# Optimization experiments

Measured on AMD Instinct MI355X. Metric: run time of the kernel, lower is better.

Reference implementation:

```python
import jax, jax.numpy as jnp
import numpy as np

LDDT_THRESHOLDS = jnp.array([0.5, 1.0, 2.0, 4.0], dtype=jnp.float32)
NUCLEIC_ACID_CUTOFF = 30.0
OTHER_CUTOFF = 15.0


def _cdist(x):
    # pairwise euclidean distances, safe sqrt (zero grad on diagonal zeros)
    sq = jnp.sum(x * x, axis=-1)                      # [b, n]
    d2 = sq[:, :, None] + sq[:, None, :] - 2.0 * jnp.einsum('bic,bjc->bij', x, x)
    d2 = jnp.maximum(d2, 0.0)
    pos = d2 > 0.0
    return jnp.where(pos, jnp.sqrt(jnp.where(pos, d2, 1.0)), 0.0)


def setup_inputs() -> dict:
    key = jax.random.key(0)
    k1, k2, k3, k4, k5 = jax.random.split(key, 5)
    b, n = 2, 4096
    true_coords = jax.random.normal(k1, (b, n, 3), dtype=jnp.float32) * 10.0
    pred_coords = true_coords + jax.random.normal(k2, (b, n, 3), dtype=jnp.float32) * 1.0
    is_dna = jax.random.bernoulli(k3, 0.25, (b, n))
    is_rna = jax.random.bernoulli(k4, 0.25, (b, n))
    coords_mask = jax.random.bernoulli(k5, 0.9, (b, n))
    return {
        'pred_coords': pred_coords,
        'true_coords': true_coords,
        'is_dna': is_dna,
        'is_rna': is_rna,
        'coords_mask': coords_mask,
    }


def reference(pred_coords, true_coords, is_dna, is_rna, coords_mask):
    b, n, _ = pred_coords.shape
    pred_dists = _cdist(pred_coords)                  # [b, n, n]
    true_dists = _cdist(true_coords)                  # [b, n, n]
    dist_diff = jnp.abs(true_dists - pred_dists)      # [b, n, n]

    # sigmoid(threshold - dist_diff), averaged over the 4 thresholds
    eps = jax.nn.sigmoid(LDDT_THRESHOLDS - dist_diff[..., None]).mean(axis=-1)  # [b, n, n]

    is_nucleotide = is_dna | is_rna                   # [b, n]
    nuc_pair = is_nucleotide[:, :, None] & is_nucleotide[:, None, :]
    inclusion_radius = jnp.where(nuc_pair,
                                 true_dists < NUCLEIC_ACID_CUTOFF,
                                 true_dists < OTHER_CUTOFF)
    mask = inclusion_radius & ~jnp.eye(n, dtype=bool)[None]
    paired_coords_mask = coords_mask[:, :, None] & coords_mask[:, None, :]
    mask = mask & paired_coords_mask

    maskf = mask.astype(eps.dtype)
    num = jnp.sum(eps * maskf, axis=(-1, -2))         # [b]
    den = jnp.maximum(jnp.sum(maskf, axis=(-1, -2)), 1.0)
    lddt = num / den
    return 1.0 - lddt.mean()
```

## Files before the change

### kernel.cpp

```cpp
#include <hip/hip_runtime.h>
#include <math.h>

#define N      4096
#define BLOCK  256
#define SEG    64
#define NITILE (N / BLOCK)
#define NJSEG  (N / SEG)
#define NTILE_TRI 544

#define PN0 4.0f
#define PN1 3.384183069f
#define PN2 0.750655861f
#define PN3 0.036699475f
#define PD1 1.128061023f
#define PD2 0.375327930f
#define PD3 0.036699475f
#define PD4 0.000553084f

__device__ __forceinline__ int tri_offset(int t) { return 66 * t - 2 * t * t; }

__global__ __launch_bounds__(BLOCK, 6) void lddt_main_kernel(
    const float* __restrict__ pred, const float* __restrict__ truec,
    const int* __restrict__ is_dna, const int* __restrict__ is_rna,
    const int* __restrict__ cmask, float* __restrict__ ws)
{
    const int L     = blockIdx.x;
    const int batch = blockIdx.z;
    const int tid   = threadIdx.x;

    int itile = 0;
#pragma unroll
    for (int u = 1; u < NITILE; ++u) itile += (L >= tri_offset(u)) ? 1 : 0;
    const int jseg = 4 * itile + (L - tri_offset(itile));
    const bool diag = (jseg >> 2) == itile;

    const int i = itile * BLOCK + tid;

    const float* pb = pred  + (size_t)batch * N * 3;
    const float* tb = truec + (size_t)batch * N * 3;
    const int* dnab = is_dna + (size_t)batch * N;
    const int* rnab = is_rna + (size_t)batch * N;
    const int* cmb  = cmask  + (size_t)batch * N;

    __shared__ float4 jP[SEG], jT[SEG];
    const int j0 = jseg * SEG;
    if (tid < SEG) {
        const int j = j0 + tid;
        jP[tid] = make_float4(pb[j*3+0], pb[j*3+1], pb[j*3+2],
                              (dnab[j] | rnab[j]) ? 15.0f : 0.0f);
        jT[tid] = make_float4(tb[j*3+0], tb[j*3+1], tb[j*3+2],
                              cmb[j] ? 1.0f : 0.0f);
    }
    __syncthreads();

    const float pix = pb[i*3+0], piy = pb[i*3+1], piz = pb[i*3+2];
    const float tix = tb[i*3+0], tiy = tb[i*3+1], tiz = tb[i*3+2];
    const float inuc01 = (dnab[i] | rnab[i]) ? 1.0f : 0.0f;
    const float icm    = cmb[i] ? 1.0f : 0.0f;

    float num = 0.0f, den = 0.0f;

#define PAIR_BODY(JJ, NEED_TRI)                                                \
    {                                                                          \
        const float4 P = jP[JJ];                                               \
        const float4 T = jT[JJ];                                               \
        float dxp = pix - P.x, dyp = piy - P.y, dzp = piz - P.z;               \
        float d2p = fmaf(dxp, dxp, fmaf(dyp, dyp, dzp * dzp));                 \
        float dp  = __builtin_amdgcn_sqrtf(d2p);                               \
        float dxt = tix - T.x, dyt = tiy - T.y, dzt = tiz - T.z;               \
        float d2t = fmaf(dxt, dxt, fmaf(dyt, dyt, dzt * dzt));                 \
        float dt  = __builtin_amdgcn_sqrtf(d2t);                               \
        float dd = fminf(fabsf(dt - dp), 20.0f);                               \
        float e  = __expf(dd);                                                 \
        float nN = fmaf(e, fmaf(e, fmaf(e, PN3, PN2), PN1), PN0);              \
        float nD = fmaf(e, fmaf(e, fmaf(e, fmaf(e, PD4, PD3), PD2), PD1), 1.0f);\
        float s  = nN * __builtin_amdgcn_rcpf(nD);                             \
        float cutoff = fmaf(inuc01, P.w, 15.0f);                               \
        bool keep = (dt < cutoff);                                             \
        if (NEED_TRI) keep = keep && (j0 + (JJ) > i);                          \
        float m = keep ? T.w : 0.0f;                                           \
        den += m;                                                              \
        num  = fmaf(m, s, num);                                                \
    }

    if (diag) {
#pragma unroll 8
        for (int jj = 0; jj < SEG; ++jj) PAIR_BODY(jj, true)
    } else {
#pragma unroll 8
        for (int jj = 0; jj < SEG; ++jj) PAIR_BODY(jj, false)
    }
#undef PAIR_BODY

    num *= 0.5f * icm;
    den *= 2.0f * icm;

    for (int off = 32; off > 0; off >>= 1) {
        num += __shfl_down(num, off);
        den += __shfl_down(den, off);
    }
    __shared__ float rn[BLOCK / 64], rd[BLOCK / 64];
    const int wid = tid >> 6, lane = tid & 63;
    if (lane == 0) { rn[wid] = num; rd[wid] = den; }
    __syncthreads();
    if (tid == 0) {
        float tn = rn[0] + rn[1] + rn[2] + rn[3];
        float td = rd[0] + rd[1] + rd[2] + rd[3];
        const int bid = batch * NTILE_TRI + L;
        ws[bid * 2 + 0] = tn;
        ws[bid * 2 + 1] = td;
    }
}

__global__ __launch_bounds__(BLOCK) void finalize_kernel(
    const float* __restrict__ ws, float* __restrict__ out, int b)
{
    __shared__ float sn[4], sd[4];
    float acc = 0.0f;
    for (int k = 0; k < b; ++k) {
        float n = 0.0f, d = 0.0f;
        for (int p = threadIdx.x; p < NTILE_TRI; p += BLOCK) {
            n += ws[(k * NTILE_TRI + p) * 2 + 0];
            d += ws[(k * NTILE_TRI + p) * 2 + 1];
        }
        for (int off = 32; off > 0; off >>= 1) {
            n += __shfl_down(n, off);
            d += __shfl_down(d, off);
        }
        if ((threadIdx.x & 63) == 0) { sn[threadIdx.x >> 6] = n; sd[threadIdx.x >> 6] = d; }
        __syncthreads();
        if (threadIdx.x == 0) {
            float tn = sn[0] + sn[1] + sn[2] + sn[3];
            float td = sd[0] + sd[1] + sd[2] + sd[3];
            acc += tn / fmaxf(td, 1.0f);
        }
        __syncthreads();
    }
    if (threadIdx.x == 0) out[0] = 1.0f - acc / (float)b;
}

extern "C" void kernel_launch(void* const* d_in, const int* in_sizes, int n_in,
                              void* d_out, int out_size, void* d_ws, size_t ws_size,
                              hipStream_t stream) {
    const float* pred  = (const float*)d_in[0];
    const float* truec = (const float*)d_in[1];
    const int* is_dna  = (const int*)d_in[2];
    const int* is_rna  = (const int*)d_in[3];
    const int* cmask   = (const int*)d_in[4];
    float* out = (float*)d_out;
    float* ws  = (float*)d_ws;

    const int b = in_sizes[2] / N;

    dim3 grid(NTILE_TRI, 1, b);
    lddt_main_kernel<<<grid, BLOCK, 0, stream>>>(pred, truec, is_dna, is_rna, cmask, ws);
    finalize_kernel<<<1, BLOCK, 0, stream>>>(ws, out, b);
}
```

Before: 86.63 us.

## Pair rcp across two entries, compare squared cutoff, halve j-segment, fuse finalize

Combines two pair sigmoid rationals under one reciprocal by cross-multiplying, which removes one rcp per pair. The radius check now compares squared distances, and the clamp is lowered to 10 to keep the product of denominators in range. The j-segment shrinks to 32, doubling the block count, and occupancy hints rise to 8. The separate finalize kernel is replaced by atomics plus a last-block reduction, with a memset added to zero the accumulators. This adds atomic contention, float atomics that make the sum order nondeterministic, and possible precision loss in the product of denominators.

```diff
diff --git a/kernel.cpp b/kernel.cpp
--- a/kernel.cpp
+++ b/kernel.cpp
@@ -3,10 +3,9 @@
 
 #define N      4096
 #define BLOCK  256
-#define SEG    64
+#define JW     32
 #define NITILE (N / BLOCK)
-#define NJSEG  (N / SEG)
-#define NTILE_TRI 544
+#define NTRI   1088
 
 #define PN0 4.0f
 #define PN1 3.384183069f
@@ -17,12 +16,16 @@
 #define PD3 0.036699475f
 #define PD4 0.000553084f
 
-__device__ __forceinline__ int tri_offset(int t) { return 66 * t - 2 * t * t; }
+#define WS_CTR   0
+#define WS_ACC   16
 
-__global__ __launch_bounds__(BLOCK, 6) void lddt_main_kernel(
+__device__ __forceinline__ int tri_off(int t) { return 132 * t - 4 * t * t; }
+
+__global__ __launch_bounds__(BLOCK, 8) void lddt_main_kernel(
     const float* __restrict__ pred, const float* __restrict__ truec,
     const int* __restrict__ is_dna, const int* __restrict__ is_rna,
-    const int* __restrict__ cmask, float* __restrict__ ws)
+    const int* __restrict__ cmask, float* __restrict__ ws,
+    float* __restrict__ out, int nblk_total, int b)
 {
     const int L     = blockIdx.x;
     const int batch = blockIdx.z;
@@ -30,9 +33,9 @@
 
     int itile = 0;
 #pragma unroll
-    for (int u = 1; u < NITILE; ++u) itile += (L >= tri_offset(u)) ? 1 : 0;
-    const int jseg = 4 * itile + (L - tri_offset(itile));
-    const bool diag = (jseg >> 2) == itile;
+    for (int u = 1; u < NITILE; ++u) itile += (L >= tri_off(u)) ? 1 : 0;
+    const int jseg = 8 * itile + (L - tri_off(itile));
+    const bool diag = (jseg < 8 * itile + 8);
 
     const int i = itile * BLOCK + tid;
 
@@ -42,12 +45,12 @@
     const int* rnab = is_rna + (size_t)batch * N;
     const int* cmb  = cmask  + (size_t)batch * N;
 
-    __shared__ float4 jP[SEG], jT[SEG];
-    const int j0 = jseg * SEG;
-    if (tid < SEG) {
+    __shared__ float4 jP[JW], jT[JW];
+    const int j0 = jseg * JW;
+    if (tid < JW) {
         const int j = j0 + tid;
         jP[tid] = make_float4(pb[j*3+0], pb[j*3+1], pb[j*3+2],
-                              (dnab[j] | rnab[j]) ? 15.0f : 0.0f);
+                              (dnab[j] | rnab[j]) ? 675.0f : 0.0f);
         jT[tid] = make_float4(tb[j*3+0], tb[j*3+1], tb[j*3+2],
                               cmb[j] ? 1.0f : 0.0f);
     }
@@ -60,37 +63,46 @@
 
     float num = 0.0f, den = 0.0f;
 
-#define PAIR_BODY(JJ, NEED_TRI)                                                \
+#define PAIR(K, NEED_TRI, NN, ND, M)                                           \
     {                                                                          \
-        const float4 P = jP[JJ];                                               \
-        const float4 T = jT[JJ];                                               \
+        const float4 P = jP[K];                                                \
+        const float4 T = jT[K];                                                \
         float dxp = pix - P.x, dyp = piy - P.y, dzp = piz - P.z;               \
         float d2p = fmaf(dxp, dxp, fmaf(dyp, dyp, dzp * dzp));                 \
         float dp  = __builtin_amdgcn_sqrtf(d2p);                               \
         float dxt = tix - T.x, dyt = tiy - T.y, dzt = tiz - T.z;               \
         float d2t = fmaf(dxt, dxt, fmaf(dyt, dyt, dzt * dzt));                 \
         float dt  = __builtin_amdgcn_sqrtf(d2t);                               \
-        float dd = fminf(fabsf(dt - dp), 20.0f);                               \
-        float e  = __expf(dd);                                                 \
-        float nN = fmaf(e, fmaf(e, fmaf(e, PN3, PN2), PN1), PN0);              \
-        float nD = fmaf(e, fmaf(e, fmaf(e, fmaf(e, PD4, PD3), PD2), PD1), 1.0f);\
-        float s  = nN * __builtin_amdgcn_rcpf(nD);                             \
-        float cutoff = fmaf(inuc01, P.w, 15.0f);                               \
-        bool keep = (dt < cutoff);                                             \
-        if (NEED_TRI) keep = keep && (j0 + (JJ) > i);                          \
-        float m = keep ? T.w : 0.0f;                                           \
-        den += m;                                                              \
-        num  = fmaf(m, s, num);                                                \
+        float dd  = fminf(fabsf(dt - dp), 10.0f);                              \
+        float e   = __expf(dd);                                                \
+        NN = fmaf(e, fmaf(e, fmaf(e, PN3, PN2), PN1), PN0);                    \
+        ND = fmaf(e, fmaf(e, fmaf(e, fmaf(e, PD4, PD3), PD2), PD1), 1.0f);     \
+        float cutsq = fmaf(inuc01, P.w, 225.0f);                               \
+        bool keep = (d2t < cutsq);                                             \
+        if (NEED_TRI) keep = keep && (j0 + (K) > i);                           \
+        M = keep ? T.w : 0.0f;                                                 \
+    }
+
+#define PAIR2(JJ, NEED_TRI)                                                    \
+    {                                                                          \
+        float n1, d1, m1, n2, d2, m2;                                          \
+        PAIR(JJ, NEED_TRI, n1, d1, m1)                                         \
+        PAIR((JJ) + 1, NEED_TRI, n2, d2, m2)                                   \
+        float t1 = m1 * n1, t2 = m2 * n2;                                      \
+        float nm = fmaf(t1, d2, t2 * d1);                                      \
+        num = fmaf(nm, __builtin_amdgcn_rcpf(d1 * d2), num);                   \
+        den += m1 + m2;                                                        \
     }
 
     if (diag) {
-#pragma unroll 8
-        for (int jj = 0; jj < SEG; ++jj) PAIR_BODY(jj, true)
+#pragma unroll 2
+        for (int jj = 0; jj < JW; jj += 2) PAIR2(jj, true)
     } else {
-#pragma unroll 8
-        for (int jj = 0; jj < SEG; ++jj) PAIR_BODY(jj, false)
+#pragma unroll 2
+        for (int jj = 0; jj < JW; jj += 2) PAIR2(jj, false)
     }
-#undef PAIR_BODY
+#undef PAIR2
+#undef PAIR
 
     num *= 0.5f * icm;
     den *= 2.0f * icm;
@@ -103,40 +115,27 @@
     const int wid = tid >> 6, lane = tid & 63;
     if (lane == 0) { rn[wid] = num; rd[wid] = den; }
     __syncthreads();
+
     if (tid == 0) {
         float tn = rn[0] + rn[1] + rn[2] + rn[3];
         float td = rd[0] + rd[1] + rd[2] + rd[3];
-        const int bid = batch * NTILE_TRI + L;
-        ws[bid * 2 + 0] = tn;
-        ws[bid * 2 + 1] = td;
+        atomicAdd(&ws[WS_ACC + 2 * batch + 0], tn);
+        atomicAdd(&ws[WS_ACC + 2 * batch + 1], td);
+        __threadfence();
+        int old = atomicAdd((int*)ws + WS_CTR, 1);
+        if (old == nblk_total - 1) {
+            __threadfence();
+            float acc = 0.0f;
+            for (int k = 0; k < b; ++k) {
+                float nm = __hip_atomic_load(&ws[WS_ACC + 2 * k + 0],
+                                             __ATOMIC_RELAXED, __HIP_MEMORY_SCOPE_AGENT);
+                float dn = __hip_atomic_load(&ws[WS_ACC + 2 * k + 1],
+                                             __ATOMIC_RELAXED, __HIP_MEMORY_SCOPE_AGENT);
+                acc += nm / fmaxf(dn, 1.0f);
+            }
+            out[0] = 1.0f - acc / (float)b;
+        }
     }
-}
-
-__global__ __launch_bounds__(BLOCK) void finalize_kernel(
-    const float* __restrict__ ws, float* __restrict__ out, int b)
-{
-    __shared__ float sn[4], sd[4];
-    float acc = 0.0f;
-    for (int k = 0; k < b; ++k) {
-        float n = 0.0f, d = 0.0f;
-        for (int p = threadIdx.x; p < NTILE_TRI; p += BLOCK) {
-            n += ws[(k * NTILE_TRI + p) * 2 + 0];
-            d += ws[(k * NTILE_TRI + p) * 2 + 1];
-        }
-        for (int off = 32; off > 0; off >>= 1) {
-            n += __shfl_down(n, off);
-            d += __shfl_down(d, off);
-        }
-        if ((threadIdx.x & 63) == 0) { sn[threadIdx.x >> 6] = n; sd[threadIdx.x >> 6] = d; }
-        __syncthreads();
-        if (threadIdx.x == 0) {
-            float tn = sn[0] + sn[1] + sn[2] + sn[3];
-            float td = sd[0] + sd[1] + sd[2] + sd[3];
-            acc += tn / fmaxf(td, 1.0f);
-        }
-        __syncthreads();
-    }
-    if (threadIdx.x == 0) out[0] = 1.0f - acc / (float)b;
 }
 
 extern "C" void kernel_launch(void* const* d_in, const int* in_sizes, int n_in,
@@ -152,7 +151,9 @@
 
     const int b = in_sizes[2] / N;
 
-    dim3 grid(NTILE_TRI, 1, b);
-    lddt_main_kernel<<<grid, BLOCK, 0, stream>>>(pred, truec, is_dna, is_rna, cmask, ws);
-    finalize_kernel<<<1, BLOCK, 0, stream>>>(ws, out, b);
+    hipMemsetAsync(ws, 0, 128, stream);
+
+    dim3 grid(NTRI, 1, b);
+    lddt_main_kernel<<<grid, BLOCK, 0, stream>>>(pred, truec, is_dna, is_rna,
+                                                 cmask, ws, out, NTRI * b, b);
 }
```

New measurement: 135.3 us. +56.1%, slower.
